# Performance work log

Measured on AMD Instinct MI355X. Metric: run time of the kernel, lower is better.

## Reference

```python
import jax, jax.numpy as jnp
import numpy as np

B = 512     # graphs
NPG = 128   # nodes per graph
EPG = 2048  # edges per graph (avg degree 16)
IN = 128
HID = 128
K = 64      # ceil(0.5 * 128), SAGPooling ratio=0.5


def setup_inputs() -> dict:
    key = jax.random.key(0)
    ks = jax.random.split(key, 8)
    n_total = B * NPG
    x = jax.random.normal(ks[0], (n_total, IN), dtype=jnp.float32)
    # intra-graph random edges (PyG batching: edges never cross graphs)
    g = jnp.repeat(jnp.arange(B, dtype=jnp.int32), EPG)
    src = g * NPG + jax.random.randint(ks[1], (B * EPG,), 0, NPG, dtype=jnp.int32)
    dst = g * NPG + jax.random.randint(ks[2], (B * EPG,), 0, NPG, dtype=jnp.int32)
    edge_index = jnp.stack([src, dst], axis=0)
    batch = jnp.repeat(jnp.arange(B, dtype=jnp.int32), NPG)
    # params (glorot-ish scaling)
    W1 = jax.random.normal(ks[3], (IN, HID), dtype=jnp.float32) / np.sqrt(IN)
    b1 = jnp.zeros((HID,), dtype=jnp.float32)
    Ws = jax.random.normal(ks[4], (HID, 1), dtype=jnp.float32) / np.sqrt(HID)
    bs = jnp.zeros((1,), dtype=jnp.float32)
    Wlin = jax.random.normal(ks[5], (HID, HID), dtype=jnp.float32) / np.sqrt(HID)
    blin = jnp.zeros((HID,), dtype=jnp.float32)
    return {"x": x, "edge_index": edge_index, "batch": batch,
            "W1": W1, "b1": b1, "Ws": Ws, "bs": bs, "Wlin": Wlin, "blin": blin}


def _gcn_conv(x, src, dst, W, b, n):
    # PyG GCNConv: add self loops, symmetric deg^-1/2 norm, aggregate src->dst
    h = x @ W  # [n, out]
    loop = jnp.arange(n, dtype=src.dtype)
    s = jnp.concatenate([src, loop])
    d = jnp.concatenate([dst, loop])
    deg = jax.ops.segment_sum(jnp.ones(d.shape[0], dtype=x.dtype), d, num_segments=n)
    norm = jax.lax.rsqrt(deg)[s] * jax.lax.rsqrt(deg)[d]  # deg >= 1 via self loops
    msg = h[s] * norm[:, None]
    return jax.ops.segment_sum(msg, d, num_segments=n) + b


def reference(x, edge_index, batch, W1, b1, Ws, bs, Wlin, blin):
    n = x.shape[0]
    src, dst = edge_index[0], edge_index[1]
    # conv1 + relu
    h = jax.nn.relu(_gcn_conv(x, src, dst, W1, b1, n))  # [n, HID]
    # SAGPooling: score via GCNConv(HID -> 1)
    score = _gcn_conv(h, src, dst, Ws, bs, n)[:, 0]  # [n]
    # per-graph top-k on raw score (graphs are uniform NPG nodes -> dense top_k)
    score2 = score.reshape(B, NPG)
    top_v, top_i = jax.lax.top_k(score2, K)  # [B, K]
    h3 = h.reshape(B, NPG, HID)
    h_kept = jnp.take_along_axis(h3, top_i[:, :, None], axis=1)  # [B, K, HID]
    h_kept = h_kept * jnp.tanh(top_v)[:, :, None]  # x[perm] * tanh(score[perm])
    # global_mean_pool over kept nodes of each graph
    pooled = h_kept.mean(axis=1)  # [B, HID]
    return pooled @ Wlin + blin
```

## Files before the change

kernel.cpp:

```cpp
#include <hip/hip_runtime.h>
#include <math.h>

#define NPG  128
#define HID  128
#define KSEL 64
#define NT   256
#define HS   132
#define AS   17
#define FS   516

typedef __attribute__((ext_vector_type(8))) __bf16 bfrag;
typedef __attribute__((ext_vector_type(4))) float f4;

static __device__ __forceinline__ __bf16 us2bf(unsigned short u) {
    union { unsigned short s; __bf16 b; } x; x.s = u; return x.b;
}
static __device__ __forceinline__ unsigned short bf2us(__bf16 b) {
    union { unsigned short s; __bf16 b; } x; x.b = b; return x.s;
}

__global__ __launch_bounds__(NT, 2) void sagpool_fused(
    const float* __restrict__ x,
    const int*   __restrict__ esrc,
    const int*   __restrict__ edst,
    const float* __restrict__ W1,
    const float* __restrict__ b1,
    const float* __restrict__ Ws,
    const float* __restrict__ bsp,
    const float* __restrict__ Wlin,
    const float* __restrict__ blin,
    float* __restrict__ out,
    int epg)
{
    __shared__ __align__(16) unsigned HpT[HID * HS];
    __shared__ __align__(16) unsigned AdjN[NPG * AS];
    __shared__ __align__(16) float rsl[NPG];
    __shared__ __align__(16) float spl[NPG];
    __shared__ __align__(16) float scl[NPG];
    __shared__ __align__(16) float wgt[NPG];
    __shared__ __align__(16) float pp[4 * HID];

    const int g = blockIdx.x, t = threadIdx.x;
    const int node0 = g * NPG;
    const long e0 = (long)g * epg;
    const int lane = t & 63, wv = t >> 6;
    const int n16 = lane & 15, quad = lane >> 4;
    const int m0 = wv * 32;

    int es[8], ed[8];
#pragma unroll
    for (int i = 0; i < 8; ++i) {
        int e = i * NT + t;
        es[i] = esrc[e0 + e] - node0;
        ed[i] = edst[e0 + e] - node0;
    }
    bfrag ah[8], al[8];
    {
        const float* xw = x + (long)(node0 + m0) * HID;
#pragma unroll
        for (int rt = 0; rt < 2; ++rt)
#pragma unroll
            for (int ks = 0; ks < 4; ++ks) {
                const float* xr = xw + (rt * 16 + n16) * HID + ks * 32 + quad * 8;
                float4 a = *reinterpret_cast<const float4*>(xr);
                float4 b = *reinterpret_cast<const float4*>(xr + 4);
                float vv[8] = {a.x, a.y, a.z, a.w, b.x, b.y, b.z, b.w};
                const int r = rt * 4 + ks;
#pragma unroll
                for (int j = 0; j < 8; ++j) {
                    __bf16 hb = (__bf16)vv[j];
                    ah[r][j] = hb;
                    al[r][j] = (__bf16)(vv[j] - (float)hb);
                }
            }
    }
    float b1v[8], wsv[8];
#pragma unroll
    for (int ct = 0; ct < 8; ++ct) {
        b1v[ct] = b1[ct * 16 + n16];
        wsv[ct] = Ws[ct * 16 + n16];
    }
    const float bsv = bsp[0];

    for (int i = t; i < NPG * AS; i += NT) AdjN[i] = 0u;
    __syncthreads();

    {
        const float4* W4 = reinterpret_cast<const float4*>(W1);
#pragma unroll
        for (int i = 0; i < 16; ++i) {
            const int fd = i * 256 + t;
            float4 w = W4[fd];
            const int dw = fd * 4;
            const int k = dw >> 7, n = dw & 127;
            const int p = (k >> 5) * 8 + (n >> 4);
            const int lane0 = ((k >> 3) & 3) * 16 + (n & 15);
            const int j = k & 7;
            unsigned* base = &HpT[p * FS + lane0 * 8 + j];
            float vv[4] = {w.x, w.y, w.z, w.w};
#pragma unroll
            for (int e = 0; e < 4; ++e) {
                __bf16 hb = (__bf16)vv[e];
                __bf16 lb = (__bf16)(vv[e] - (float)hb);
                base[e * 8] = ((unsigned)bf2us(hb) << 16) | (unsigned)bf2us(lb);
            }
        }
    }
#pragma unroll
    for (int i = 0; i < 8; ++i)
        atomicAdd(&AdjN[ed[i] * AS + (es[i] >> 3)], 1u << ((es[i] & 7) * 4));
    __syncthreads();

    if (t < NPG) {
        unsigned* row = &AdjN[t * AS];
        unsigned sum = 0;
#pragma unroll
        for (int w = 0; w < 16; ++w) {
            unsigned u = row[w];
            unsigned b = (u & 0x0F0F0F0Fu) + ((u >> 4) & 0x0F0F0F0Fu);
            sum += (b * 0x01010101u) >> 24;
        }
        rsl[t] = rsqrtf((float)(sum + 1));
        row[t >> 3] += 1u << ((t & 7) * 4);
    }

    f4 acc[2][8];
#pragma unroll
    for (int rt = 0; rt < 2; ++rt)
#pragma unroll
        for (int ct = 0; ct < 8; ++ct) {
            acc[rt][ct].x = 0.f; acc[rt][ct].y = 0.f;
            acc[rt][ct].z = 0.f; acc[rt][ct].w = 0.f;
        }
#pragma unroll
    for (int ks = 0; ks < 4; ++ks)
#pragma unroll
        for (int ct = 0; ct < 8; ++ct) {
            const unsigned* fp = &HpT[(ks * 8 + ct) * FS + lane * 8];
            uint4 a0 = *reinterpret_cast<const uint4*>(fp);
            uint4 a1 = *reinterpret_cast<const uint4*>(fp + 4);
            unsigned ww[8] = {a0.x, a0.y, a0.z, a0.w, a1.x, a1.y, a1.z, a1.w};
            bfrag bh, bl;
#pragma unroll
            for (int j = 0; j < 8; ++j) {
                bh[j] = us2bf((unsigned short)(ww[j] >> 16));
                bl[j] = us2bf((unsigned short)(ww[j] & 0xFFFFu));
            }
#pragma unroll
            for (int rt = 0; rt < 2; ++rt) {
                const int r = rt * 4 + ks;
                acc[rt][ct] = __builtin_amdgcn_mfma_f32_16x16x32_bf16(ah[r], bh, acc[rt][ct], 0, 0, 0);
                acc[rt][ct] = __builtin_amdgcn_mfma_f32_16x16x32_bf16(al[r], bh, acc[rt][ct], 0, 0, 0);
                acc[rt][ct] = __builtin_amdgcn_mfma_f32_16x16x32_bf16(ah[r], bl, acc[rt][ct], 0, 0, 0);
                acc[rt][ct] = __builtin_amdgcn_mfma_f32_16x16x32_bf16(al[r], bl, acc[rt][ct], 0, 0, 0);
            }
        }
    __syncthreads();

#pragma unroll
    for (int rt = 0; rt < 2; ++rt) {
        const int mb = m0 + rt * 16 + quad * 4;
        f4 rs4 = *reinterpret_cast<const f4*>(&rsl[mb]);
#pragma unroll
        for (int ct = 0; ct < 8; ++ct) {
            uint4 st;
            unsigned pw[4];
#pragma unroll
            for (int reg = 0; reg < 4; ++reg) {
                float v = acc[rt][ct][reg] * rs4[reg];
                __bf16 hb = (__bf16)v;
                __bf16 lb = (__bf16)(v - (float)hb);
                pw[reg] = ((unsigned)bf2us(hb) << 16) | (unsigned)bf2us(lb);
            }
            st.x = pw[0]; st.y = pw[1]; st.z = pw[2]; st.w = pw[3];
            *reinterpret_cast<uint4*>(&HpT[(ct * 16 + n16) * HS + mb]) = st;
        }
    }
    __syncthreads();

    f4 hacc[2][8];
#pragma unroll
    for (int mt = 0; mt < 2; ++mt)
#pragma unroll
        for (int ct = 0; ct < 8; ++ct) {
            hacc[mt][ct].x = 0.f; hacc[mt][ct].y = 0.f;
            hacc[mt][ct].z = 0.f; hacc[mt][ct].w = 0.f;
        }
#pragma unroll
    for (int ks = 0; ks < 4; ++ks) {
        bfrag af[2];
#pragma unroll
        for (int mt = 0; mt < 2; ++mt) {
            unsigned w = AdjN[(m0 + mt * 16 + n16) * AS + ks * 4 + quad];
#pragma unroll
            for (int j = 0; j < 8; ++j)
                af[mt][j] = (__bf16)(float)((w >> (4 * j)) & 15u);
        }
#pragma unroll
        for (int ct = 0; ct < 8; ++ct) {
            const unsigned* bp = &HpT[(ct * 16 + n16) * HS + ks * 32 + quad * 8];
            uint4 w0 = *reinterpret_cast<const uint4*>(bp);
            uint4 w1 = *reinterpret_cast<const uint4*>(bp + 4);
            unsigned ww[8] = {w0.x, w0.y, w0.z, w0.w, w1.x, w1.y, w1.z, w1.w};
            bfrag bh, bl;
#pragma unroll
            for (int j = 0; j < 8; ++j) {
                bh[j] = us2bf((unsigned short)(ww[j] >> 16));
                bl[j] = us2bf((unsigned short)(ww[j] & 0xFFFFu));
            }
#pragma unroll
            for (int mt = 0; mt < 2; ++mt) {
                hacc[mt][ct] = __builtin_amdgcn_mfma_f32_16x16x32_bf16(af[mt], bh, hacc[mt][ct], 0, 0, 0);
                hacc[mt][ct] = __builtin_amdgcn_mfma_f32_16x16x32_bf16(af[mt], bl, hacc[mt][ct], 0, 0, 0);
            }
        }
    }

    f4 rsm[2];
#pragma unroll
    for (int mt = 0; mt < 2; ++mt)
        rsm[mt] = *reinterpret_cast<const f4*>(&rsl[m0 + mt * 16 + quad * 4]);
#pragma unroll
    for (int mt = 0; mt < 2; ++mt)
#pragma unroll
        for (int ct = 0; ct < 8; ++ct)
#pragma unroll
            for (int reg = 0; reg < 4; ++reg)
                hacc[mt][ct][reg] = fmaxf(hacc[mt][ct][reg] * rsm[mt][reg] + b1v[ct], 0.f);

    {
        float dot[2][4];
#pragma unroll
        for (int mt = 0; mt < 2; ++mt)
#pragma unroll
            for (int reg = 0; reg < 4; ++reg) dot[mt][reg] = 0.f;
#pragma unroll
        for (int ct = 0; ct < 8; ++ct)
#pragma unroll
            for (int mt = 0; mt < 2; ++mt)
#pragma unroll
                for (int reg = 0; reg < 4; ++reg)
                    dot[mt][reg] += hacc[mt][ct][reg] * wsv[ct];
#pragma unroll
        for (int d = 1; d < 16; d <<= 1)
#pragma unroll
            for (int mt = 0; mt < 2; ++mt)
#pragma unroll
                for (int reg = 0; reg < 4; ++reg)
                    dot[mt][reg] += __shfl_xor(dot[mt][reg], d, 64);
        if (n16 == 0) {
#pragma unroll
            for (int mt = 0; mt < 2; ++mt)
#pragma unroll
                for (int reg = 0; reg < 4; ++reg)
                    spl[m0 + mt * 16 + quad * 4 + reg] = rsm[mt][reg] * dot[mt][reg];
        }
    }
    __syncthreads();

    if (t < NPG) {
        const unsigned* row = &AdjN[t * AS];
        float sc = 0.f;
#pragma unroll
        for (int w = 0; w < 16; ++w) {
            unsigned u = row[w];
            const float* sp = &spl[w * 8];
            sc += (float)(u & 15u)         * sp[0] + (float)((u >> 4)  & 15u) * sp[1]
                + (float)((u >> 8)  & 15u) * sp[2] + (float)((u >> 12) & 15u) * sp[3]
                + (float)((u >> 16) & 15u) * sp[4] + (float)((u >> 20) & 15u) * sp[5]
                + (float)((u >> 24) & 15u) * sp[6] + (float)(u >> 28)         * sp[7];
        }
        scl[t] = rsl[t] * sc + bsv;
    }
    __syncthreads();

    if (t < NPG) {
        float v = scl[t];
        int rank = 0;
#pragma unroll
        for (int j4 = 0; j4 < 32; ++j4) {
            float4 u = *reinterpret_cast<const float4*>(&scl[j4 * 4]);
            const int jb = j4 * 4;
            rank += (u.x > v || (u.x == v && jb     < t)) ? 1 : 0;
            rank += (u.y > v || (u.y == v && jb + 1 < t)) ? 1 : 0;
            rank += (u.z > v || (u.z == v && jb + 2 < t)) ? 1 : 0;
            rank += (u.w > v || (u.w == v && jb + 3 < t)) ? 1 : 0;
        }
        wgt[t] = (rank < KSEL) ? tanhf(v) * (1.0f / KSEL) : 0.f;
    }
    __syncthreads();

    {
        float p[8];
        f4 wm[2];
#pragma unroll
        for (int mt = 0; mt < 2; ++mt)
            wm[mt] = *reinterpret_cast<const f4*>(&wgt[m0 + mt * 16 + quad * 4]);
#pragma unroll
        for (int ct = 0; ct < 8; ++ct) {
            float s = 0.f;
#pragma unroll
            for (int mt = 0; mt < 2; ++mt)
#pragma unroll
                for (int reg = 0; reg < 4; ++reg)
                    s += wm[mt][reg] * hacc[mt][ct][reg];
            p[ct] = s;
        }
#pragma unroll
        for (int d = 16; d < 64; d <<= 1)
#pragma unroll
            for (int ct = 0; ct < 8; ++ct)
                p[ct] += __shfl_xor(p[ct], d, 64);
        if (quad == 0) {
#pragma unroll
            for (int ct = 0; ct < 8; ++ct)
                pp[wv * HID + ct * 16 + n16] = p[ct];
        }
    }
    __syncthreads();
    if (t < NPG)
        scl[t] = pp[t] + pp[HID + t] + pp[2 * HID + t] + pp[3 * HID + t];
    __syncthreads();

    {
        const int c = t & 127, hf = t >> 7;
        float s = 0.f;
#pragma unroll 8
        for (int k = hf * 64; k < hf * 64 + 64; ++k)
            s += scl[k] * Wlin[k * HID + c];
        pp[t] = s;
    }
    __syncthreads();
    if (t < NPG)
        out[(long)g * HID + t] = pp[t] + pp[t + 128] + blin[t];
}

extern "C" void kernel_launch(void* const* d_in, const int* in_sizes, int n_in,
                              void* d_out, int out_size, void* d_ws, size_t ws_size,
                              hipStream_t stream) {
    const float* x    = (const float*)d_in[0];
    const int*   ei   = (const int*)  d_in[1];
    const float* W1   = (const float*)d_in[3];
    const float* b1   = (const float*)d_in[4];
    const float* Ws   = (const float*)d_in[5];
    const float* bs   = (const float*)d_in[6];
    const float* Wlin = (const float*)d_in[7];
    const float* blin = (const float*)d_in[8];
    float* out = (float*)d_out;

    const int E = in_sizes[1] / 2;
    const int nnodes = in_sizes[0] / HID;
    const int B = nnodes / NPG;
    const int epg = E / B;

    sagpool_fused<<<B, NT, 0, stream>>>(x, ei, ei + E, W1, b1, Ws, bs,
                                        Wlin, blin, out, epg);
}
```

Measured before the change: 111.7 us.

## Vectorize W1 staging, drop lo*lo MFMA term, stage Wlin in LDS

```diff
diff --git a/kernel.cpp b/kernel.cpp
--- a/kernel.cpp
+++ b/kernel.cpp
@@ -17,6 +17,11 @@
 }
 static __device__ __forceinline__ unsigned short bf2us(__bf16 b) {
     union { unsigned short s; __bf16 b; } x; x.b = b; return x.s;
+}
+static __device__ __forceinline__ unsigned packhl(float v) {
+    __bf16 hb = (__bf16)v;
+    __bf16 lb = (__bf16)(v - (float)hb);
+    return ((unsigned)bf2us(hb) << 16) | (unsigned)bf2us(lb);
 }
 
 __global__ __launch_bounds__(NT, 2) void sagpool_fused(
@@ -86,23 +91,27 @@
     __syncthreads();
 
     {
-        const float4* W4 = reinterpret_cast<const float4*>(W1);
-#pragma unroll
-        for (int i = 0; i < 16; ++i) {
-            const int fd = i * 256 + t;
-            float4 w = W4[fd];
-            const int dw = fd * 4;
-            const int k = dw >> 7, n = dw & 127;
-            const int p = (k >> 5) * 8 + (n >> 4);
-            const int lane0 = ((k >> 3) & 3) * 16 + (n & 15);
-            const int j = k & 7;
-            unsigned* base = &HpT[p * FS + lane0 * 8 + j];
-            float vv[4] = {w.x, w.y, w.z, w.w};
-#pragma unroll
-            for (int e = 0; e < 4; ++e) {
-                __bf16 hb = (__bf16)vv[e];
-                __bf16 lb = (__bf16)(vv[e] - (float)hb);
-                base[e * 8] = ((unsigned)bf2us(hb) << 16) | (unsigned)bf2us(lb);
+#pragma unroll
+        for (int i = 0; i < 4; ++i) {
+            const int tau = i * NT + t;
+            const int ng = tau & 31, kg = tau >> 5;
+            const int n0 = ng * 4, k0 = kg * 4;
+            f4 r[4];
+#pragma unroll
+            for (int e = 0; e < 4; ++e)
+                r[e] = *reinterpret_cast<const f4*>(W1 + (k0 + e) * HID + n0);
+            const int p  = (k0 >> 5) * 8 + (n0 >> 4);
+            const int j0 = k0 & 7;
+            const int l0 = ((k0 >> 3) & 3) * 16;
+#pragma unroll
+            for (int c = 0; c < 4; ++c) {
+                const int lane0 = l0 + ((n0 + c) & 15);
+                uint4 st;
+                st.x = packhl(r[0][c]);
+                st.y = packhl(r[1][c]);
+                st.z = packhl(r[2][c]);
+                st.w = packhl(r[3][c]);
+                *reinterpret_cast<uint4*>(&HpT[p * FS + lane0 * 8 + j0]) = st;
             }
         }
     }
@@ -152,7 +161,6 @@
                 acc[rt][ct] = __builtin_amdgcn_mfma_f32_16x16x32_bf16(ah[r], bh, acc[rt][ct], 0, 0, 0);
                 acc[rt][ct] = __builtin_amdgcn_mfma_f32_16x16x32_bf16(al[r], bh, acc[rt][ct], 0, 0, 0);
                 acc[rt][ct] = __builtin_amdgcn_mfma_f32_16x16x32_bf16(ah[r], bl, acc[rt][ct], 0, 0, 0);
-                acc[rt][ct] = __builtin_amdgcn_mfma_f32_16x16x32_bf16(al[r], bl, acc[rt][ct], 0, 0, 0);
             }
         }
     __syncthreads();
@@ -166,12 +174,8 @@
             uint4 st;
             unsigned pw[4];
 #pragma unroll
-            for (int reg = 0; reg < 4; ++reg) {
-                float v = acc[rt][ct][reg] * rs4[reg];
-                __bf16 hb = (__bf16)v;
-                __bf16 lb = (__bf16)(v - (float)hb);
-                pw[reg] = ((unsigned)bf2us(hb) << 16) | (unsigned)bf2us(lb);
-            }
+            for (int reg = 0; reg < 4; ++reg)
+                pw[reg] = packhl(acc[rt][ct][reg] * rs4[reg]);
             st.x = pw[0]; st.y = pw[1]; st.z = pw[2]; st.w = pw[3];
             *reinterpret_cast<uint4*>(&HpT[(ct * 16 + n16) * HS + mb]) = st;
         }
@@ -271,6 +275,18 @@
                 + (float)((u >> 24) & 15u) * sp[6] + (float)(u >> 28)         * sp[7];
         }
         scl[t] = rsl[t] * sc + bsv;
+    } else {
+        const int tt = t - NPG;
+        const f4* WL4 = reinterpret_cast<const f4*>(Wlin);
+        for (int ib = 0; ib < 4; ++ib) {
+            f4 w[8];
+#pragma unroll
+            for (int u = 0; u < 8; ++u)
+                w[u] = WL4[(ib * 8 + u) * 128 + tt];
+#pragma unroll
+            for (int u = 0; u < 8; ++u)
+                *reinterpret_cast<f4*>(&HpT[((ib * 8 + u) * 128 + tt) * 4]) = w[u];
+        }
     }
     __syncthreads();
 
@@ -323,16 +339,27 @@
     __syncthreads();
 
     {
-        const int c = t & 127, hf = t >> 7;
-        float s = 0.f;
+        const int c4 = (t & 31) * 4, rg = t >> 5;
+        f4 s4; s4.x = 0.f; s4.y = 0.f; s4.z = 0.f; s4.w = 0.f;
 #pragma unroll 8
-        for (int k = hf * 64; k < hf * 64 + 64; ++k)
-            s += scl[k] * Wlin[k * HID + c];
-        pp[t] = s;
-    }
-    __syncthreads();
-    if (t < NPG)
-        out[(long)g * HID + t] = pp[t] + pp[t + 128] + blin[t];
+        for (int kk = 0; kk < 16; ++kk) {
+            const int k = rg * 16 + kk;
+            const f4 w = *reinterpret_cast<const f4*>(&HpT[k * HID + c4]);
+            const float sk = scl[k];
+            s4.x += sk * w.x; s4.y += sk * w.y;
+            s4.z += sk * w.z; s4.w += sk * w.w;
+        }
+        float* part = reinterpret_cast<float*>(AdjN);
+        *reinterpret_cast<f4*>(&part[rg * HID + c4]) = s4;
+    }
+    __syncthreads();
+    if (t < NPG) {
+        const float* part = reinterpret_cast<const float*>(AdjN);
+        float s = blin[t];
+#pragma unroll
+        for (int r = 0; r < 8; ++r) s += part[r * HID + t];
+        out[(long)g * HID + t] = s;
+    }
 }
 
 extern "C" void kernel_launch(void* const* d_in, const int* in_sizes, int n_in,
```

After: 110.5 us. Within noise of the previous version (-1.2%).
